# Optimization experiments

Measured on AMD Instinct MI355X. Metric: run time of the kernel, lower is better.

The kernel has to match this reference:

```python
import jax, jax.numpy as jnp
import numpy as np

N, E, G = 10000, 160000, 64
F, C1, C2, C3, K, NC = 128, 128, 256, 512, 5, 10


def setup_inputs() -> dict:
    key = jax.random.key(0)
    ks = jax.random.split(key, 12)
    s = 0.05
    return {
        "x": jax.random.normal(ks[0], (N, F), dtype=jnp.float32),
        "edge_index": jax.random.randint(ks[1], (2, E), 0, N, dtype=jnp.int64),
        "batch": jnp.sort(jax.random.randint(ks[2], (N,), 0, G, dtype=jnp.int64)),
        "W_cheb": jax.random.normal(ks[3], (K, F, C1), dtype=jnp.float32) * s,
        "b_cheb": jnp.zeros((C1,), jnp.float32),
        "W_g1": jax.random.normal(ks[4], (C1, C2), dtype=jnp.float32) * s,
        "b_g1": jnp.zeros((C2,), jnp.float32),
        "W_g2": jax.random.normal(ks[5], (C2, C3), dtype=jnp.float32) * s,
        "b_g2": jnp.zeros((C3,), jnp.float32),
        "w_gate": jax.random.normal(ks[6], (C3, 1), dtype=jnp.float32) * s,
        "b_gate": jnp.zeros((1,), jnp.float32),
        "W_fc": jax.random.normal(ks[7], (C3, NC), dtype=jnp.float32) * s,
        "b_fc": jnp.zeros((NC,), jnp.float32),
    }


def _deg_inv_sqrt(deg):
    return jnp.where(deg > 0, jax.lax.rsqrt(jnp.maximum(deg, 1e-12)), 0.0)


def cheb_conv(x, src, dst, W, b):
    # PyG ChebConv, sym normalization, lambda_max=2 => scaled Laplacian = -D^-1/2 A D^-1/2
    ones = jnp.ones((src.shape[0],), x.dtype)
    deg = jax.ops.segment_sum(ones, src, num_segments=N)
    dinv = _deg_inv_sqrt(deg)
    w = -(dinv[src] * dinv[dst])  # [E]

    def prop(h):
        return jax.ops.segment_sum(w[:, None] * h[src], dst, num_segments=N)

    tx0 = x
    tx1 = prop(x)
    out = tx0 @ W[0] + tx1 @ W[1]
    for k in range(2, W.shape[0]):
        tx2 = 2.0 * prop(tx1) - tx0
        out = out + tx2 @ W[k]
        tx0, tx1 = tx1, tx2
    return out + b


def gcn_conv(x, src, dst, W, b):
    # PyG GCNConv: add self-loops, sym norm D~^-1/2 (A+I) D~^-1/2, transform then aggregate
    loop = jnp.arange(N, dtype=src.dtype)
    src_a = jnp.concatenate([src, loop])
    dst_a = jnp.concatenate([dst, loop])
    ones = jnp.ones((src_a.shape[0],), x.dtype)
    deg = jax.ops.segment_sum(ones, dst_a, num_segments=N)
    dinv = _deg_inv_sqrt(deg)
    norm = dinv[src_a] * dinv[dst_a]  # [E+N]
    h = x @ W
    return jax.ops.segment_sum(norm[:, None] * h[src_a], dst_a, num_segments=N) + b


def attention_pool(x, batch, w_gate, b_gate):
    logits = (x @ w_gate + b_gate)[:, 0]  # [N]
    m = jax.ops.segment_max(logits, batch, num_segments=G)
    e = jnp.exp(logits - m[batch])
    s = jax.ops.segment_sum(e, batch, num_segments=G)
    alpha = e / s[batch]
    return jax.ops.segment_sum(alpha[:, None] * x, batch, num_segments=G)  # [G, C3]


def reference(x, edge_index, batch, W_cheb, b_cheb, W_g1, b_g1, W_g2, b_g2,
              w_gate, b_gate, W_fc, b_fc):
    src, dst = edge_index[0], edge_index[1]
    h = jax.nn.relu(cheb_conv(x, src, dst, W_cheb, b_cheb))
    h = jax.nn.relu(gcn_conv(h, src, dst, W_g1, b_g1))
    h = jax.nn.relu(gcn_conv(h, src, dst, W_g2, b_g2))
    g = attention_pool(h, batch, w_gate, b_gate)
    logits = g @ W_fc + b_fc
    return jax.nn.log_softmax(logits, axis=1)
```

## Files before the change

### kernel.cpp

```cpp
#include <hip/hip_runtime.h>
#include <hip/hip_bf16.h>
#include <math.h>

#define N_NODES 10000
#define N_EDGES 160000
#define N_GRAPHS 64
#define F_IN    128
#define C1_DIM  128
#define C2_DIM  256
#define C3_DIM  512
#define K_CHEB  5
#define NCLS    10
#define TC      (K_CHEB * F_IN)

typedef short v8s __attribute__((ext_vector_type(8)));
typedef float v4f __attribute__((ext_vector_type(4)));

static __device__ __forceinline__ unsigned short f2bf(float f) {
    unsigned u = __float_as_uint(f);
    unsigned r = (u + 0x7FFFu + ((u >> 16) & 1u)) >> 16;
    return (unsigned short)r;
}
static __device__ __forceinline__ float bf_lo(unsigned u) { return __uint_as_float(u << 16); }
static __device__ __forceinline__ float bf_hi(unsigned u) { return __uint_as_float(u & 0xFFFF0000u); }

#define PREP_A (N_NODES * 32)
#define PREP_B (TC * C1_DIM)
#define PREP_C (C1_DIM * C2_DIM)
#define PREP_D (C2_DIM * C3_DIM)
#define PREP_E N_NODES
#define PREP_F N_NODES
#define PREP_H (N_GRAPHS * C3_DIM)
#define PREP_G N_EDGES
#define PREP_TOTAL (PREP_A + PREP_B + PREP_C + PREP_D + PREP_E + PREP_F + PREP_H + PREP_G)
__global__ void prep_kernel(const float* __restrict__ x, unsigned short* __restrict__ tcat,
                            const float* __restrict__ Wcheb, unsigned short* __restrict__ Wcb_t,
                            const float* __restrict__ Wg1, unsigned short* __restrict__ Wg1_t,
                            const float* __restrict__ Wg2, unsigned short* __restrict__ Wg2_t,
                            const int* __restrict__ batch, int* __restrict__ gptr,
                            float* __restrict__ logits, float* __restrict__ pooled,
                            const int* __restrict__ src, const int* __restrict__ dst,
                            int* __restrict__ cnt_s, int* __restrict__ cnt_d) {
    int id = blockIdx.x * blockDim.x + threadIdx.x;
    if (id < PREP_A) {
        int n = id >> 5, f = (id & 31) * 4;
        float4 v = *(const float4*)(x + (size_t)n * F_IN + f);
        ushort4 o; o.x = f2bf(v.x); o.y = f2bf(v.y); o.z = f2bf(v.z); o.w = f2bf(v.w);
        *(ushort4*)(tcat + (size_t)n * TC + f) = o;
        return;
    }
    id -= PREP_A;
    if (id < PREP_B) {
        int k = id % TC, n = id / TC;
        Wcb_t[(size_t)n * TC + k] = f2bf(Wcheb[(size_t)k * C1_DIM + n]);
        return;
    }
    id -= PREP_B;
    if (id < PREP_C) {
        int k = id % C1_DIM, n = id / C1_DIM;
        Wg1_t[(size_t)n * C1_DIM + k] = f2bf(Wg1[(size_t)k * C2_DIM + n]);
        return;
    }
    id -= PREP_C;
    if (id < PREP_D) {
        int k = id % C2_DIM, n = id / C2_DIM;
        Wg2_t[(size_t)n * C2_DIM + k] = f2bf(Wg2[(size_t)k * C3_DIM + n]);
        return;
    }
    id -= PREP_D;
    if (id < PREP_E) {
        int i = id;
        int b = batch[i];
        if (i == 0) { for (int g = 0; g <= b; g++) gptr[g] = 0; }
        else {
            int bp = batch[i - 1];
            for (int g = bp + 1; g <= b; g++) gptr[g] = i;
        }
        if (i == N_NODES - 1) { for (int g = b + 1; g <= N_GRAPHS; g++) gptr[g] = N_NODES; }
        return;
    }
    id -= PREP_E;
    if (id < PREP_F) { logits[id] = 0.0f; return; }
    id -= PREP_F;
    if (id < PREP_H) { pooled[id] = 0.0f; return; }
    id -= PREP_H;
    if (id < PREP_G) {
        atomicAdd(&cnt_s[src[id]], 1);
        atomicAdd(&cnt_d[dst[id]], 1);
    }
}

__global__ __launch_bounds__(256) void scan_kernel(const int* __restrict__ cnt_d,
                                                   int* __restrict__ rowptr, int n) {
    __shared__ int ldsc[N_NODES];
    __shared__ int sums[256];
    int tid = threadIdx.x;
    for (int i = tid; i < n; i += 256) ldsc[i] = cnt_d[i];
    __syncthreads();
    int chunk = (n + 255) / 256;
    int s0 = min(n, tid * chunk), s1 = min(n, s0 + chunk);
    int loc = 0;
    for (int i = s0; i < s1; i++) loc += ldsc[i];
    sums[tid] = loc;
    __syncthreads();
    for (int off = 1; off < 256; off <<= 1) {
        int t = (tid >= off) ? sums[tid - off] : 0;
        __syncthreads();
        sums[tid] += t;
        __syncthreads();
    }
    int pre = sums[tid] - loc;
    for (int i = s0; i < s1; i++) { int v = ldsc[i]; ldsc[i] = pre; pre += v; }
    __syncthreads();
    for (int i = tid; i < n; i += 256) rowptr[i] = ldsc[i];
    if (tid == 255) rowptr[n] = pre;
}

__global__ void fill_kernel(const int* __restrict__ src, const int* __restrict__ dst,
                            const int* __restrict__ cnt_s, const int* __restrict__ cnt_d,
                            const int* __restrict__ rowptr, int* __restrict__ fillc,
                            int2* __restrict__ ecb, int2* __restrict__ egc, int E) {
    int e = blockIdx.x * blockDim.x + threadIdx.x;
    if (e >= E) return;
    int s = src[e], d = dst[e];
    int pos = rowptr[d] + atomicAdd(&fillc[d], 1);
    int cs = cnt_s[s], cd = cnt_s[d];
    float ds = (cs > 0) ? rsqrtf((float)cs) : 0.0f;
    float dd = (cd > 0) ? rsqrtf((float)cd) : 0.0f;
    float nr = rsqrtf((float)cnt_d[s] + 1.0f) * rsqrtf((float)cnt_d[d] + 1.0f);
    ecb[pos] = make_int2(s, __float_as_int(-(ds * dd)));
    egc[pos] = make_int2(s, __float_as_int(nr));
}

__global__ __launch_bounds__(256) void gather_cheb_bf(
        const unsigned short* __restrict__ tb, const int* __restrict__ rowptr,
        const int2* __restrict__ edges,
        const unsigned short* __restrict__ base, float alpha, float beta,
        unsigned short* __restrict__ outc, int n) {
    int w = (blockIdx.x * blockDim.x + threadIdx.x) >> 6;
    int lane = threadIdx.x & 63;
    if (w >= n) return;
    float a0 = 0.0f, a1 = 0.0f;
    int rs = rowptr[w], re = rowptr[w + 1];
    for (int b = rs; b < re; b += 64) {
        int cl = 0; float wl = 0.0f;
        if (b + lane < re) { int2 e = edges[b + lane]; cl = e.x; wl = __int_as_float(e.y); }
        int nk16 = (min(64, re - b) + 15) & ~15;
        for (int j = 0; j < nk16; j += 16) {
            int ss[16]; float ww[16]; unsigned uu[16];
            #pragma unroll
            for (int q = 0; q < 16; q++) { ss[q] = __shfl(cl, j + q); ww[q] = __shfl(wl, j + q); }
            #pragma unroll
            for (int q = 0; q < 16; q++) uu[q] = ((const unsigned*)(tb + (size_t)ss[q] * TC))[lane];
            #pragma unroll
            for (int q = 0; q < 16; q++) { a0 += ww[q] * bf_lo(uu[q]); a1 += ww[q] * bf_hi(uu[q]); }
        }
    }
    if (base) {
        unsigned ub = ((const unsigned*)(base + (size_t)w * TC))[lane];
        a0 = alpha * a0 + beta * bf_lo(ub);
        a1 = alpha * a1 + beta * bf_hi(ub);
    } else {
        a0 *= alpha; a1 *= alpha;
    }
    ushort2 o; o.x = f2bf(a0); o.y = f2bf(a1);
    *(ushort2*)(outc + (size_t)w * TC + lane * 2) = o;
}

template<int FPL>
__global__ __launch_bounds__(256) void gather_gcn_pre(
        const unsigned short* __restrict__ tb, const int* __restrict__ rowptr,
        const int2* __restrict__ edges,
        const int* __restrict__ cnt_d, unsigned short* __restrict__ z, int n) {
    const int C = FPL * 64;
    int w = (blockIdx.x * blockDim.x + threadIdx.x) >> 6;
    int lane = threadIdx.x & 63;
    if (w >= n) return;
    float acc[FPL];
    #pragma unroll
    for (int q = 0; q < FPL; q++) acc[q] = 0.0f;
    int rs = rowptr[w], re = rowptr[w + 1];
    for (int b = rs; b < re; b += 64) {
        int cl = 0; float wl = 0.0f;
        if (b + lane < re) { int2 e = edges[b + lane]; cl = e.x; wl = __int_as_float(e.y); }
        int nk16 = (min(64, re - b) + 15) & ~15;
        for (int j = 0; j < nk16; j += 16) {
            int ss[16]; float ww[16];
            #pragma unroll
            for (int q = 0; q < 16; q++) { ss[q] = __shfl(cl, j + q); ww[q] = __shfl(wl, j + q); }
            if constexpr (FPL == 2) {
                unsigned uu[16];
                #pragma unroll
                for (int q = 0; q < 16; q++) uu[q] = ((const unsigned*)(tb + (size_t)ss[q] * C))[lane];
                #pragma unroll
                for (int q = 0; q < 16; q++) { acc[0] += ww[q] * bf_lo(uu[q]); acc[1] += ww[q] * bf_hi(uu[q]); }
            } else {
                uint2 uu[16];
                #pragma unroll
                for (int q = 0; q < 16; q++) uu[q] = ((const uint2*)(tb + (size_t)ss[q] * C))[lane];
                #pragma unroll
                for (int q = 0; q < 16; q++) {
                    acc[0] += ww[q] * bf_lo(uu[q].x); acc[1] += ww[q] * bf_hi(uu[q].x);
                    acc[2] += ww[q] * bf_lo(uu[q].y); acc[3] += ww[q] * bf_hi(uu[q].y);
                }
            }
        }
    }
    float sn = 1.0f / (float)(cnt_d[w] + 1);
    if constexpr (FPL == 2) {
        unsigned u = ((const unsigned*)(tb + (size_t)w * C))[lane];
        acc[0] += sn * bf_lo(u); acc[1] += sn * bf_hi(u);
        ushort2 o; o.x = f2bf(acc[0]); o.y = f2bf(acc[1]);
        *(ushort2*)(z + (size_t)w * C + lane * 2) = o;
    } else {
        uint2 u = ((const uint2*)(tb + (size_t)w * C))[lane];
        acc[0] += sn * bf_lo(u.x); acc[1] += sn * bf_hi(u.x);
        acc[2] += sn * bf_lo(u.y); acc[3] += sn * bf_hi(u.y);
        ushort4 o; o.x = f2bf(acc[0]); o.y = f2bf(acc[1]);
        o.z = f2bf(acc[2]); o.w = f2bf(acc[3]);
        *(ushort4*)(z + (size_t)w * C + lane * 4) = o;
    }
}

template<int JT, int KC>
__global__ __launch_bounds__(256) void gemm_bf16(
        const unsigned short* __restrict__ A, const unsigned short* __restrict__ Bt,
        const float* __restrict__ bias,
        unsigned short* __restrict__ Cb, const float* __restrict__ wg,
        float* __restrict__ logits, int M, int N) {
    int m0 = blockIdx.y * 64, n0 = blockIdx.x * (JT * 32);
    int wave = threadIdx.x >> 6, lane = threadIdx.x & 63;
    int wm = (wave & 1) * 32, wn = (wave >> 1) * (JT * 16);
    int l15 = lane & 15, quad = lane >> 4;

    v4f acc[2][JT];
    #pragma unroll
    for (int i = 0; i < 2; i++)
        #pragma unroll
        for (int j = 0; j < JT; j++) acc[i][j] = (v4f){0.f, 0.f, 0.f, 0.f};

    const unsigned short* Ab[2]; bool av[2];
    #pragma unroll
    for (int i = 0; i < 2; i++) {
        int row = m0 + wm + i * 16 + l15;
        av[i] = row < M;
        Ab[i] = A + (size_t)(av[i] ? row : 0) * KC + quad * 8;
    }
    const unsigned short* Bb[JT];
    #pragma unroll
    for (int j = 0; j < JT; j++) {
        int coln = n0 + wn + j * 16 + l15;
        Bb[j] = Bt + (size_t)coln * KC + quad * 8;
    }
    const v8s zero8 = {0, 0, 0, 0, 0, 0, 0, 0};

    #pragma unroll
    for (int k0 = 0; k0 < KC; k0 += 32) {
        v8s a[2], b[JT];
        #pragma unroll
        for (int i = 0; i < 2; i++) a[i] = av[i] ? *(const v8s*)(Ab[i] + k0) : zero8;
        #pragma unroll
        for (int j = 0; j < JT; j++) b[j] = *(const v8s*)(Bb[j] + k0);
        #pragma unroll
        for (int i = 0; i < 2; i++)
            #pragma unroll
            for (int j = 0; j < JT; j++)
                acc[i][j] = __builtin_amdgcn_mfma_f32_16x16x32_bf16(a[i], b[j], acc[i][j], 0, 0, 0);
    }

    float bv[JT], wgj[JT];
    #pragma unroll
    for (int j = 0; j < JT; j++) {
        int coln = n0 + wn + j * 16 + l15;
        bv[j] = bias[coln];
        wgj[j] = wg ? wg[coln] : 0.0f;
    }
    #pragma unroll
    for (int i = 0; i < 2; i++) {
        #pragma unroll
        for (int r = 0; r < 4; r++) {
            int row = m0 + wm + i * 16 + quad * 4 + r;
            if (row >= M) continue;
            float gval = 0.0f;
            #pragma unroll
            for (int j = 0; j < JT; j++) {
                int coln = n0 + wn + j * 16 + l15;
                float v = fmaxf(acc[i][j][r] + bv[j], 0.0f);
                Cb[(size_t)row * N + coln] = f2bf(v);
                gval += v * wgj[j];
            }
            if (wg) {
                #pragma unroll
                for (int off = 1; off < 16; off <<= 1) gval += __shfl_xor(gval, off);
                if (l15 == 0) atomicAdd(&logits[row], gval);
            }
        }
    }
}

__global__ __launch_bounds__(256) void pool_partial(const unsigned short* __restrict__ h3b,
        const float* __restrict__ logits, const int* __restrict__ gptr,
        float* __restrict__ pooled) {
    __shared__ float red[256];
    int g = blockIdx.x, sl = blockIdx.y, tid = threadIdx.x;
    int gs = gptr[g], ge = gptr[g + 1];
    float m = -INFINITY;
    for (int i = gs + tid; i < ge; i += 256) m = fmaxf(m, logits[i]);
    red[tid] = m; __syncthreads();
    for (int off = 128; off > 0; off >>= 1) {
        if (tid < off) red[tid] = fmaxf(red[tid], red[tid + off]);
        __syncthreads();
    }
    m = red[0]; __syncthreads();
    float s = 0.0f;
    for (int i = gs + tid; i < ge; i += 256) s += expf(logits[i] - m);
    red[tid] = s; __syncthreads();
    for (int off = 128; off > 0; off >>= 1) {
        if (tid < off) red[tid] += red[tid + off];
        __syncthreads();
    }
    s = red[0];
    float sinv = (s > 0.0f) ? 1.0f / s : 0.0f;
    int cnt = ge - gs;
    int i0 = gs + (cnt * sl) / 8;
    int i1 = gs + (cnt * (sl + 1)) / 8;
    float a0 = 0.0f, a1 = 0.0f;
    for (int i = i0; i < i1; i++) {
        float al = expf(logits[i] - m) * sinv;
        unsigned u = ((const unsigned*)(h3b + (size_t)i * C3_DIM))[tid];
        a0 += al * bf_lo(u);
        a1 += al * bf_hi(u);
    }
    if (i1 > i0) {
        atomicAdd(&pooled[(size_t)g * C3_DIM + tid * 2 + 0], a0);
        atomicAdd(&pooled[(size_t)g * C3_DIM + tid * 2 + 1], a1);
    }
}

__global__ void fc_kernel(const float* __restrict__ pooled, const float* __restrict__ Wfc,
                          const float* __restrict__ bfc, float* __restrict__ out) {
    int g = blockIdx.x;
    int t = threadIdx.x;
    float acc = -INFINITY;
    if (t < NCLS) {
        acc = bfc[t];
        for (int k = 0; k < C3_DIM; k++)
            acc += pooled[(size_t)g * C3_DIM + k] * Wfc[k * NCLS + t];
    }
    float m = acc;
    #pragma unroll
    for (int off = 8; off > 0; off >>= 1) m = fmaxf(m, __shfl_xor(m, off, 16));
    float e = (t < NCLS) ? expf(acc - m) : 0.0f;
    float s = e;
    #pragma unroll
    for (int off = 8; off > 0; off >>= 1) s += __shfl_xor(s, off, 16);
    if (t < NCLS) out[g * NCLS + t] = acc - m - logf(s);
}

extern "C" void kernel_launch(void* const* d_in, const int* in_sizes, int n_in,
                              void* d_out, int out_size, void* d_ws, size_t ws_size,
                              hipStream_t stream) {
    const float* x      = (const float*)d_in[0];
    const int*   ei     = (const int*)d_in[1];
    const int*   batch  = (const int*)d_in[2];
    const float* W_cheb = (const float*)d_in[3];
    const float* b_cheb = (const float*)d_in[4];
    const float* W_g1   = (const float*)d_in[5];
    const float* b_g1   = (const float*)d_in[6];
    const float* W_g2   = (const float*)d_in[7];
    const float* b_g2   = (const float*)d_in[8];
    const float* w_gate = (const float*)d_in[9];
    const float* W_fc   = (const float*)d_in[11];
    const float* b_fc   = (const float*)d_in[12];
    const int* src = ei;
    const int* dst = ei + N_EDGES;
    float* out = (float*)d_out;

    const int N = N_NODES, E = N_EDGES, G = N_GRAPHS;

    char* Wp = (char*)d_ws;
    auto alloc = [&](size_t bytes) {
        void* p = Wp;
        Wp += (bytes + 255) & ~(size_t)255;
        return p;
    };
    int*   cnt3    = (int*)alloc((size_t)3 * N * 4);
    int*   cnt_s   = cnt3;
    int*   cnt_d   = cnt3 + N;
    int*   fillc   = cnt3 + 2 * N;
    int*   rowptr  = (int*)alloc((N + 1) * 4);
    int2*  ecb     = (int2*)alloc((size_t)E * 8);
    int2*  egc     = (int2*)alloc((size_t)E * 8);
    unsigned short* tcat  = (unsigned short*)alloc((size_t)N * TC * 2);
    unsigned short* h1b   = (unsigned short*)alloc((size_t)N * C1_DIM * 2);
    unsigned short* z1b   = (unsigned short*)alloc((size_t)N * C1_DIM * 2);
    unsigned short* h2b   = (unsigned short*)alloc((size_t)N * C2_DIM * 2);
    unsigned short* z2b   = (unsigned short*)alloc((size_t)N * C2_DIM * 2);
    unsigned short* h3b   = (unsigned short*)alloc((size_t)N * C3_DIM * 2);
    unsigned short* Wcb_t = (unsigned short*)alloc((size_t)TC * C1_DIM * 2);
    unsigned short* Wg1_t = (unsigned short*)alloc((size_t)C1_DIM * C2_DIM * 2);
    unsigned short* Wg2_t = (unsigned short*)alloc((size_t)C2_DIM * C3_DIM * 2);
    float* logits  = (float*)alloc(N * 4);
    int*   gptr    = (int*)alloc((G + 1) * 4);
    float* pooled  = (float*)alloc((size_t)G * C3_DIM * 4);

    dim3 blk(256);
    auto cdiv = [](int a, int b) { return (a + b - 1) / b; };

    hipMemsetAsync(cnt3, 0, (size_t)3 * N * sizeof(int), stream);
    hipLaunchKernelGGL(prep_kernel, dim3(cdiv(PREP_TOTAL, 256)), blk, 0, stream,
                       x, tcat, W_cheb, Wcb_t, W_g1, Wg1_t, W_g2, Wg2_t,
                       batch, gptr, logits, pooled, src, dst, cnt_s, cnt_d);

    hipLaunchKernelGGL(scan_kernel, dim3(1), blk, 0, stream, cnt_d, rowptr, N);
    hipLaunchKernelGGL(fill_kernel, dim3(cdiv(E, 256)), blk, 0, stream,
                       src, dst, cnt_s, cnt_d, rowptr, fillc, ecb, egc, E);

    const int NWB = cdiv(N, 4);

    hipLaunchKernelGGL(gather_cheb_bf, dim3(NWB), blk, 0, stream,
                       tcat + 0 * F_IN, rowptr, ecb,
                       (const unsigned short*)nullptr, 1.0f, 0.0f, tcat + 1 * F_IN, N);
    hipLaunchKernelGGL(gather_cheb_bf, dim3(NWB), blk, 0, stream,
                       tcat + 1 * F_IN, rowptr, ecb,
                       tcat + 0 * F_IN, 2.0f, -1.0f, tcat + 2 * F_IN, N);
    hipLaunchKernelGGL(gather_cheb_bf, dim3(NWB), blk, 0, stream,
                       tcat + 2 * F_IN, rowptr, ecb,
                       tcat + 1 * F_IN, 2.0f, -1.0f, tcat + 3 * F_IN, N);
    hipLaunchKernelGGL(gather_cheb_bf, dim3(NWB), blk, 0, stream,
                       tcat + 3 * F_IN, rowptr, ecb,
                       tcat + 2 * F_IN, 2.0f, -1.0f, tcat + 4 * F_IN, N);

    hipLaunchKernelGGL((gemm_bf16<2, TC>), dim3(C1_DIM / 64, cdiv(N, 64)), blk, 0, stream,
                       tcat, Wcb_t, b_cheb, h1b,
                       (const float*)nullptr, (float*)nullptr, N, C1_DIM);

    hipLaunchKernelGGL(gather_gcn_pre<2>, dim3(NWB), blk, 0, stream,
                       h1b, rowptr, egc, cnt_d, z1b, N);
    hipLaunchKernelGGL((gemm_bf16<4, C1_DIM>), dim3(C2_DIM / 128, cdiv(N, 64)), blk, 0, stream,
                       z1b, Wg1_t, b_g1, h2b,
                       (const float*)nullptr, (float*)nullptr, N, C2_DIM);

    hipLaunchKernelGGL(gather_gcn_pre<4>, dim3(NWB), blk, 0, stream,
                       h2b, rowptr, egc, cnt_d, z2b, N);
    hipLaunchKernelGGL((gemm_bf16<4, C2_DIM>), dim3(C3_DIM / 128, cdiv(N, 64)), blk, 0, stream,
                       z2b, Wg2_t, b_g2, h3b,
                       w_gate, logits, N, C3_DIM);

    hipLaunchKernelGGL(pool_partial, dim3(G, 8), blk, 0, stream, h3b, logits, gptr, pooled);
    hipLaunchKernelGGL(fc_kernel, dim3(G), dim3(64), 0, stream, pooled, W_fc, b_fc, out);
}
```

Measured before the change: 264.1 us.

## Fuse graph gathers into following GEMMs via LDS and merge pool with FC

Each aggregation step (the last Chebyshev propagation and both GCN neighbour sums) now runs inside the GEMM kernel that consumes it. The aggregated 64-row tile is written to LDS and fed to the MFMA loop from there, so the intermediate z1/z2 buffers and the fourth Chebyshev slice never go to global memory. Attention pooling and the FC/log-softmax are merged into one kernel with one block per graph, which removes the pooled atomics and their zeroing. In exchange each GEMM block now covers the full output width and does the irregular gather serially per wave, giving fewer blocks (157) and lower parallelism, and the pooling no longer splits a graph's nodes across 8 blocks.

```diff
diff --git a/kernel.cpp b/kernel.cpp
--- a/kernel.cpp
+++ b/kernel.cpp
@@ -12,6 +12,8 @@
 #define K_CHEB  5
 #define NCLS    10
 #define TC      (K_CHEB * F_IN)
+#define LDSW1   136
+#define LDSW2   264
 
 typedef short v8s __attribute__((ext_vector_type(8)));
 typedef float v4f __attribute__((ext_vector_type(4)));
@@ -30,15 +32,14 @@
 #define PREP_D (C2_DIM * C3_DIM)
 #define PREP_E N_NODES
 #define PREP_F N_NODES
-#define PREP_H (N_GRAPHS * C3_DIM)
 #define PREP_G N_EDGES
-#define PREP_TOTAL (PREP_A + PREP_B + PREP_C + PREP_D + PREP_E + PREP_F + PREP_H + PREP_G)
+#define PREP_TOTAL (PREP_A + PREP_B + PREP_C + PREP_D + PREP_E + PREP_F + PREP_G)
 __global__ void prep_kernel(const float* __restrict__ x, unsigned short* __restrict__ tcat,
                             const float* __restrict__ Wcheb, unsigned short* __restrict__ Wcb_t,
                             const float* __restrict__ Wg1, unsigned short* __restrict__ Wg1_t,
                             const float* __restrict__ Wg2, unsigned short* __restrict__ Wg2_t,
                             const int* __restrict__ batch, int* __restrict__ gptr,
-                            float* __restrict__ logits, float* __restrict__ pooled,
+                            float* __restrict__ logits,
                             const int* __restrict__ src, const int* __restrict__ dst,
                             int* __restrict__ cnt_s, int* __restrict__ cnt_d) {
     int id = blockIdx.x * blockDim.x + threadIdx.x;
@@ -82,8 +83,6 @@
     id -= PREP_E;
     if (id < PREP_F) { logits[id] = 0.0f; return; }
     id -= PREP_F;
-    if (id < PREP_H) { pooled[id] = 0.0f; return; }
-    id -= PREP_H;
     if (id < PREP_G) {
         atomicAdd(&cnt_s[src[id]], 1);
         atomicAdd(&cnt_d[dst[id]], 1);
@@ -167,113 +166,256 @@
     *(ushort2*)(outc + (size_t)w * TC + lane * 2) = o;
 }
 
-template<int FPL>
-__global__ __launch_bounds__(256) void gather_gcn_pre(
-        const unsigned short* __restrict__ tb, const int* __restrict__ rowptr,
-        const int2* __restrict__ edges,
-        const int* __restrict__ cnt_d, unsigned short* __restrict__ z, int n) {
-    const int C = FPL * 64;
-    int w = (blockIdx.x * blockDim.x + threadIdx.x) >> 6;
-    int lane = threadIdx.x & 63;
-    if (w >= n) return;
-    float acc[FPL];
-    #pragma unroll
-    for (int q = 0; q < FPL; q++) acc[q] = 0.0f;
-    int rs = rowptr[w], re = rowptr[w + 1];
-    for (int b = rs; b < re; b += 64) {
-        int cl = 0; float wl = 0.0f;
-        if (b + lane < re) { int2 e = edges[b + lane]; cl = e.x; wl = __int_as_float(e.y); }
-        int nk16 = (min(64, re - b) + 15) & ~15;
-        for (int j = 0; j < nk16; j += 16) {
-            int ss[16]; float ww[16];
-            #pragma unroll
-            for (int q = 0; q < 16; q++) { ss[q] = __shfl(cl, j + q); ww[q] = __shfl(wl, j + q); }
-            if constexpr (FPL == 2) {
-                unsigned uu[16];
-                #pragma unroll
-                for (int q = 0; q < 16; q++) uu[q] = ((const unsigned*)(tb + (size_t)ss[q] * C))[lane];
-                #pragma unroll
-                for (int q = 0; q < 16; q++) { acc[0] += ww[q] * bf_lo(uu[q]); acc[1] += ww[q] * bf_hi(uu[q]); }
-            } else {
-                uint2 uu[16];
-                #pragma unroll
-                for (int q = 0; q < 16; q++) uu[q] = ((const uint2*)(tb + (size_t)ss[q] * C))[lane];
-                #pragma unroll
-                for (int q = 0; q < 16; q++) {
-                    acc[0] += ww[q] * bf_lo(uu[q].x); acc[1] += ww[q] * bf_hi(uu[q].x);
-                    acc[2] += ww[q] * bf_lo(uu[q].y); acc[3] += ww[q] * bf_hi(uu[q].y);
+__global__ __launch_bounds__(256) void cheb4_gemm1(
+        const unsigned short* __restrict__ tcat, const int* __restrict__ rowptr,
+        const int2* __restrict__ ecb, const unsigned short* __restrict__ Bt,
+        const float* __restrict__ bias, unsigned short* __restrict__ h1b, int M) {
+    __shared__ unsigned short ldsA[64 * LDSW1];
+    int tid = threadIdx.x, wave = tid >> 6, lane = tid & 63;
+    int m0 = blockIdx.x * 64;
+    const unsigned short* t3 = tcat + 3 * F_IN;
+    const unsigned short* t2 = tcat + 2 * F_IN;
+
+    for (int na = wave * 16; na < wave * 16 + 16; na++) {
+        int w = m0 + na;
+        float a0 = 0.0f, a1 = 0.0f;
+        if (w < M) {
+            int rs = rowptr[w], re = rowptr[w + 1];
+            for (int b = rs; b < re; b += 64) {
+                int cl = 0; float wl = 0.0f;
+                if (b + lane < re) { int2 e = ecb[b + lane]; cl = e.x; wl = __int_as_float(e.y); }
+                int nk16 = (min(64, re - b) + 15) & ~15;
+                for (int j = 0; j < nk16; j += 16) {
+                    int ss[16]; float ww[16]; unsigned uu[16];
+                    #pragma unroll
+                    for (int q = 0; q < 16; q++) { ss[q] = __shfl(cl, j + q); ww[q] = __shfl(wl, j + q); }
+                    #pragma unroll
+                    for (int q = 0; q < 16; q++) uu[q] = ((const unsigned*)(t3 + (size_t)ss[q] * TC))[lane];
+                    #pragma unroll
+                    for (int q = 0; q < 16; q++) { a0 += ww[q] * bf_lo(uu[q]); a1 += ww[q] * bf_hi(uu[q]); }
                 }
             }
-        }
-    }
-    float sn = 1.0f / (float)(cnt_d[w] + 1);
-    if constexpr (FPL == 2) {
-        unsigned u = ((const unsigned*)(tb + (size_t)w * C))[lane];
-        acc[0] += sn * bf_lo(u); acc[1] += sn * bf_hi(u);
-        ushort2 o; o.x = f2bf(acc[0]); o.y = f2bf(acc[1]);
-        *(ushort2*)(z + (size_t)w * C + lane * 2) = o;
-    } else {
-        uint2 u = ((const uint2*)(tb + (size_t)w * C))[lane];
-        acc[0] += sn * bf_lo(u.x); acc[1] += sn * bf_hi(u.x);
-        acc[2] += sn * bf_lo(u.y); acc[3] += sn * bf_hi(u.y);
-        ushort4 o; o.x = f2bf(acc[0]); o.y = f2bf(acc[1]);
-        o.z = f2bf(acc[2]); o.w = f2bf(acc[3]);
-        *(ushort4*)(z + (size_t)w * C + lane * 4) = o;
-    }
-}
-
-template<int JT, int KC>
-__global__ __launch_bounds__(256) void gemm_bf16(
-        const unsigned short* __restrict__ A, const unsigned short* __restrict__ Bt,
-        const float* __restrict__ bias,
-        unsigned short* __restrict__ Cb, const float* __restrict__ wg,
-        float* __restrict__ logits, int M, int N) {
-    int m0 = blockIdx.y * 64, n0 = blockIdx.x * (JT * 32);
-    int wave = threadIdx.x >> 6, lane = threadIdx.x & 63;
-    int wm = (wave & 1) * 32, wn = (wave >> 1) * (JT * 16);
+            unsigned ub = ((const unsigned*)(t2 + (size_t)w * TC))[lane];
+            a0 = 2.0f * a0 - bf_lo(ub);
+            a1 = 2.0f * a1 - bf_hi(ub);
+        }
+        ushort2 o; o.x = f2bf(a0); o.y = f2bf(a1);
+        *(ushort2*)(ldsA + na * LDSW1 + lane * 2) = o;
+    }
+    __syncthreads();
+
+    int wm = (wave & 1) * 32, wn = (wave >> 1) * 64;
     int l15 = lane & 15, quad = lane >> 4;
-
-    v4f acc[2][JT];
+    v4f acc[2][4];
     #pragma unroll
     for (int i = 0; i < 2; i++)
         #pragma unroll
-        for (int j = 0; j < JT; j++) acc[i][j] = (v4f){0.f, 0.f, 0.f, 0.f};
-
-    const unsigned short* Ab[2]; bool av[2];
+        for (int j = 0; j < 4; j++) acc[i][j] = (v4f){0.f, 0.f, 0.f, 0.f};
+    const unsigned short* Ab[2]; bool av[2]; int rl[2];
     #pragma unroll
     for (int i = 0; i < 2; i++) {
         int row = m0 + wm + i * 16 + l15;
         av[i] = row < M;
-        Ab[i] = A + (size_t)(av[i] ? row : 0) * KC + quad * 8;
-    }
-    const unsigned short* Bb[JT];
-    #pragma unroll
-    for (int j = 0; j < JT; j++) {
-        int coln = n0 + wn + j * 16 + l15;
-        Bb[j] = Bt + (size_t)coln * KC + quad * 8;
+        Ab[i] = tcat + (size_t)(av[i] ? row : 0) * TC + quad * 8;
+        rl[i] = wm + i * 16 + l15;
+    }
+    const unsigned short* Bb[4];
+    #pragma unroll
+    for (int j = 0; j < 4; j++) {
+        int coln = wn + j * 16 + l15;
+        Bb[j] = Bt + (size_t)coln * TC + quad * 8;
     }
     const v8s zero8 = {0, 0, 0, 0, 0, 0, 0, 0};
-
-    #pragma unroll
-    for (int k0 = 0; k0 < KC; k0 += 32) {
-        v8s a[2], b[JT];
-        #pragma unroll
-        for (int i = 0; i < 2; i++) a[i] = av[i] ? *(const v8s*)(Ab[i] + k0) : zero8;
-        #pragma unroll
-        for (int j = 0; j < JT; j++) b[j] = *(const v8s*)(Bb[j] + k0);
+    #pragma unroll
+    for (int k0 = 0; k0 < TC; k0 += 32) {
+        v8s a[2], b[4];
+        #pragma unroll
+        for (int i = 0; i < 2; i++) {
+            if (k0 < 4 * F_IN) a[i] = av[i] ? *(const v8s*)(Ab[i] + k0) : zero8;
+            else               a[i] = *(const v8s*)(ldsA + rl[i] * LDSW1 + (k0 - 4 * F_IN) + quad * 8);
+        }
+        #pragma unroll
+        for (int j = 0; j < 4; j++) b[j] = *(const v8s*)(Bb[j] + k0);
         #pragma unroll
         for (int i = 0; i < 2; i++)
             #pragma unroll
-            for (int j = 0; j < JT; j++)
+            for (int j = 0; j < 4; j++)
                 acc[i][j] = __builtin_amdgcn_mfma_f32_16x16x32_bf16(a[i], b[j], acc[i][j], 0, 0, 0);
     }
-
-    float bv[JT], wgj[JT];
-    #pragma unroll
-    for (int j = 0; j < JT; j++) {
-        int coln = n0 + wn + j * 16 + l15;
+    #pragma unroll
+    for (int j = 0; j < 4; j++) {
+        int coln = wn + j * 16 + l15;
+        float bv = bias[coln];
+        #pragma unroll
+        for (int i = 0; i < 2; i++) {
+            #pragma unroll
+            for (int r = 0; r < 4; r++) {
+                int row = m0 + wm + i * 16 + quad * 4 + r;
+                if (row >= M) continue;
+                float v = fmaxf(acc[i][j][r] + bv, 0.0f);
+                h1b[(size_t)row * C1_DIM + coln] = f2bf(v);
+            }
+        }
+    }
+}
+
+__global__ __launch_bounds__(256) void gcn_gemm2(
+        const unsigned short* __restrict__ h1b, const int* __restrict__ rowptr,
+        const int2* __restrict__ egc, const int* __restrict__ cnt_d,
+        const unsigned short* __restrict__ Bt, const float* __restrict__ bias,
+        unsigned short* __restrict__ h2b, int M) {
+    __shared__ unsigned short ldsA[64 * LDSW1];
+    int tid = threadIdx.x, wave = tid >> 6, lane = tid & 63;
+    int m0 = blockIdx.x * 64;
+
+    for (int na = wave * 16; na < wave * 16 + 16; na++) {
+        int w = m0 + na;
+        float a0 = 0.0f, a1 = 0.0f;
+        if (w < M) {
+            int rs = rowptr[w], re = rowptr[w + 1];
+            for (int b = rs; b < re; b += 64) {
+                int cl = 0; float wl = 0.0f;
+                if (b + lane < re) { int2 e = egc[b + lane]; cl = e.x; wl = __int_as_float(e.y); }
+                int nk16 = (min(64, re - b) + 15) & ~15;
+                for (int j = 0; j < nk16; j += 16) {
+                    int ss[16]; float ww[16]; unsigned uu[16];
+                    #pragma unroll
+                    for (int q = 0; q < 16; q++) { ss[q] = __shfl(cl, j + q); ww[q] = __shfl(wl, j + q); }
+                    #pragma unroll
+                    for (int q = 0; q < 16; q++) uu[q] = ((const unsigned*)(h1b + (size_t)ss[q] * C1_DIM))[lane];
+                    #pragma unroll
+                    for (int q = 0; q < 16; q++) { a0 += ww[q] * bf_lo(uu[q]); a1 += ww[q] * bf_hi(uu[q]); }
+                }
+            }
+            float sn = 1.0f / (float)(cnt_d[w] + 1);
+            unsigned u = ((const unsigned*)(h1b + (size_t)w * C1_DIM))[lane];
+            a0 += sn * bf_lo(u);
+            a1 += sn * bf_hi(u);
+        }
+        ushort2 o; o.x = f2bf(a0); o.y = f2bf(a1);
+        *(ushort2*)(ldsA + na * LDSW1 + lane * 2) = o;
+    }
+    __syncthreads();
+
+    int wm = (wave & 1) * 32, wn = (wave >> 1) * 128;
+    int l15 = lane & 15, quad = lane >> 4;
+    v4f acc[2][8];
+    #pragma unroll
+    for (int i = 0; i < 2; i++)
+        #pragma unroll
+        for (int j = 0; j < 8; j++) acc[i][j] = (v4f){0.f, 0.f, 0.f, 0.f};
+    int rl[2] = {wm + l15, wm + 16 + l15};
+    const unsigned short* Bb[8];
+    #pragma unroll
+    for (int j = 0; j < 8; j++) {
+        int coln = wn + j * 16 + l15;
+        Bb[j] = Bt + (size_t)coln * C1_DIM + quad * 8;
+    }
+    #pragma unroll
+    for (int k0 = 0; k0 < C1_DIM; k0 += 32) {
+        v8s a[2], b[8];
+        #pragma unroll
+        for (int i = 0; i < 2; i++) a[i] = *(const v8s*)(ldsA + rl[i] * LDSW1 + k0 + quad * 8);
+        #pragma unroll
+        for (int j = 0; j < 8; j++) b[j] = *(const v8s*)(Bb[j] + k0);
+        #pragma unroll
+        for (int i = 0; i < 2; i++)
+            #pragma unroll
+            for (int j = 0; j < 8; j++)
+                acc[i][j] = __builtin_amdgcn_mfma_f32_16x16x32_bf16(a[i], b[j], acc[i][j], 0, 0, 0);
+    }
+    #pragma unroll
+    for (int j = 0; j < 8; j++) {
+        int coln = wn + j * 16 + l15;
+        float bv = bias[coln];
+        #pragma unroll
+        for (int i = 0; i < 2; i++) {
+            #pragma unroll
+            for (int r = 0; r < 4; r++) {
+                int row = m0 + wm + i * 16 + quad * 4 + r;
+                if (row >= M) continue;
+                float v = fmaxf(acc[i][j][r] + bv, 0.0f);
+                h2b[(size_t)row * C2_DIM + coln] = f2bf(v);
+            }
+        }
+    }
+}
+
+__global__ __launch_bounds__(512) void gcn_gemm3(
+        const unsigned short* __restrict__ h2b, const int* __restrict__ rowptr,
+        const int2* __restrict__ egc, const int* __restrict__ cnt_d,
+        const unsigned short* __restrict__ Bt, const float* __restrict__ bias,
+        const float* __restrict__ wg, unsigned short* __restrict__ h3b,
+        float* __restrict__ logits, int M) {
+    __shared__ unsigned short ldsA[64 * LDSW2];
+    int tid = threadIdx.x, wave = tid >> 6, lane = tid & 63;
+    int m0 = blockIdx.x * 64;
+
+    for (int na = wave * 8; na < wave * 8 + 8; na++) {
+        int w = m0 + na;
+        float a0 = 0.0f, a1 = 0.0f, a2 = 0.0f, a3 = 0.0f;
+        if (w < M) {
+            int rs = rowptr[w], re = rowptr[w + 1];
+            for (int b = rs; b < re; b += 64) {
+                int cl = 0; float wl = 0.0f;
+                if (b + lane < re) { int2 e = egc[b + lane]; cl = e.x; wl = __int_as_float(e.y); }
+                int nk16 = (min(64, re - b) + 15) & ~15;
+                for (int j = 0; j < nk16; j += 16) {
+                    int ss[16]; float ww[16]; uint2 uu[16];
+                    #pragma unroll
+                    for (int q = 0; q < 16; q++) { ss[q] = __shfl(cl, j + q); ww[q] = __shfl(wl, j + q); }
+                    #pragma unroll
+                    for (int q = 0; q < 16; q++) uu[q] = ((const uint2*)(h2b + (size_t)ss[q] * C2_DIM))[lane];
+                    #pragma unroll
+                    for (int q = 0; q < 16; q++) {
+                        a0 += ww[q] * bf_lo(uu[q].x); a1 += ww[q] * bf_hi(uu[q].x);
+                        a2 += ww[q] * bf_lo(uu[q].y); a3 += ww[q] * bf_hi(uu[q].y);
+                    }
+                }
+            }
+            float sn = 1.0f / (float)(cnt_d[w] + 1);
+            uint2 u = ((const uint2*)(h2b + (size_t)w * C2_DIM))[lane];
+            a0 += sn * bf_lo(u.x); a1 += sn * bf_hi(u.x);
+            a2 += sn * bf_lo(u.y); a3 += sn * bf_hi(u.y);
+        }
+        ushort4 o; o.x = f2bf(a0); o.y = f2bf(a1); o.z = f2bf(a2); o.w = f2bf(a3);
+        *(ushort4*)(ldsA + na * LDSW2 + lane * 4) = o;
+    }
+    __syncthreads();
+
+    int wm = (wave >> 2) * 32, wn = (wave & 3) * 128;
+    int l15 = lane & 15, quad = lane >> 4;
+    v4f acc[2][8];
+    #pragma unroll
+    for (int i = 0; i < 2; i++)
+        #pragma unroll
+        for (int j = 0; j < 8; j++) acc[i][j] = (v4f){0.f, 0.f, 0.f, 0.f};
+    int rl[2] = {wm + l15, wm + 16 + l15};
+    const unsigned short* Bb[8];
+    #pragma unroll
+    for (int j = 0; j < 8; j++) {
+        int coln = wn + j * 16 + l15;
+        Bb[j] = Bt + (size_t)coln * C2_DIM + quad * 8;
+    }
+    #pragma unroll
+    for (int k0 = 0; k0 < C2_DIM; k0 += 32) {
+        v8s a[2], b[8];
+        #pragma unroll
+        for (int i = 0; i < 2; i++) a[i] = *(const v8s*)(ldsA + rl[i] * LDSW2 + k0 + quad * 8);
+        #pragma unroll
+        for (int j = 0; j < 8; j++) b[j] = *(const v8s*)(Bb[j] + k0);
+        #pragma unroll
+        for (int i = 0; i < 2; i++)
+            #pragma unroll
+            for (int j = 0; j < 8; j++)
+                acc[i][j] = __builtin_amdgcn_mfma_f32_16x16x32_bf16(a[i], b[j], acc[i][j], 0, 0, 0);
+    }
+    float bv[8], wgj[8];
+    #pragma unroll
+    for (int j = 0; j < 8; j++) {
+        int coln = wn + j * 16 + l15;
         bv[j] = bias[coln];
-        wgj[j] = wg ? wg[coln] : 0.0f;
+        wgj[j] = wg[coln];
     }
     #pragma unroll
     for (int i = 0; i < 2; i++) {
@@ -283,26 +425,26 @@
             if (row >= M) continue;
             float gval = 0.0f;
             #pragma unroll
-            for (int j = 0; j < JT; j++) {
-                int coln = n0 + wn + j * 16 + l15;
+            for (int j = 0; j < 8; j++) {
+                int coln = wn + j * 16 + l15;
                 float v = fmaxf(acc[i][j][r] + bv[j], 0.0f);
-                Cb[(size_t)row * N + coln] = f2bf(v);
+                h3b[(size_t)row * C3_DIM + coln] = f2bf(v);
                 gval += v * wgj[j];
             }
-            if (wg) {
-                #pragma unroll
-                for (int off = 1; off < 16; off <<= 1) gval += __shfl_xor(gval, off);
-                if (l15 == 0) atomicAdd(&logits[row], gval);
-            }
-        }
-    }
-}
-
-__global__ __launch_bounds__(256) void pool_partial(const unsigned short* __restrict__ h3b,
+            #pragma unroll
+            for (int off = 1; off < 16; off <<= 1) gval += __shfl_xor(gval, off);
+            if (l15 == 0) atomicAdd(&logits[row], gval);
+        }
+    }
+}
+
+__global__ __launch_bounds__(256) void pool_fc(const unsigned short* __restrict__ h3b,
         const float* __restrict__ logits, const int* __restrict__ gptr,
-        float* __restrict__ pooled) {
+        const float* __restrict__ Wfc, const float* __restrict__ bfc,
+        float* __restrict__ out) {
     __shared__ float red[256];
-    int g = blockIdx.x, sl = blockIdx.y, tid = threadIdx.x;
+    __shared__ float plds[C3_DIM];
+    int g = blockIdx.x, tid = threadIdx.x;
     int gs = gptr[g], ge = gptr[g + 1];
     float m = -INFINITY;
     for (int i = gs + tid; i < ge; i += 256) m = fmaxf(m, logits[i]);
@@ -321,40 +463,32 @@
     }
     s = red[0];
     float sinv = (s > 0.0f) ? 1.0f / s : 0.0f;
-    int cnt = ge - gs;
-    int i0 = gs + (cnt * sl) / 8;
-    int i1 = gs + (cnt * (sl + 1)) / 8;
     float a0 = 0.0f, a1 = 0.0f;
-    for (int i = i0; i < i1; i++) {
+    for (int i = gs; i < ge; i++) {
         float al = expf(logits[i] - m) * sinv;
         unsigned u = ((const unsigned*)(h3b + (size_t)i * C3_DIM))[tid];
         a0 += al * bf_lo(u);
         a1 += al * bf_hi(u);
     }
-    if (i1 > i0) {
-        atomicAdd(&pooled[(size_t)g * C3_DIM + tid * 2 + 0], a0);
-        atomicAdd(&pooled[(size_t)g * C3_DIM + tid * 2 + 1], a1);
-    }
-}
-
-__global__ void fc_kernel(const float* __restrict__ pooled, const float* __restrict__ Wfc,
-                          const float* __restrict__ bfc, float* __restrict__ out) {
-    int g = blockIdx.x;
-    int t = threadIdx.x;
-    float acc = -INFINITY;
-    if (t < NCLS) {
-        acc = bfc[t];
-        for (int k = 0; k < C3_DIM; k++)
-            acc += pooled[(size_t)g * C3_DIM + k] * Wfc[k * NCLS + t];
-    }
-    float m = acc;
-    #pragma unroll
-    for (int off = 8; off > 0; off >>= 1) m = fmaxf(m, __shfl_xor(m, off, 16));
-    float e = (t < NCLS) ? expf(acc - m) : 0.0f;
-    float s = e;
-    #pragma unroll
-    for (int off = 8; off > 0; off >>= 1) s += __shfl_xor(s, off, 16);
-    if (t < NCLS) out[g * NCLS + t] = acc - m - logf(s);
+    plds[tid * 2 + 0] = a0;
+    plds[tid * 2 + 1] = a1;
+    __syncthreads();
+    if (tid < 16) {
+        float acc = -INFINITY;
+        if (tid < NCLS) {
+            acc = bfc[tid];
+            for (int k = 0; k < C3_DIM; k++)
+                acc += plds[k] * Wfc[k * NCLS + tid];
+        }
+        float mm = acc;
+        #pragma unroll
+        for (int off = 8; off > 0; off >>= 1) mm = fmaxf(mm, __shfl_xor(mm, off, 16));
+        float e = (tid < NCLS) ? expf(acc - mm) : 0.0f;
+        float ss = e;
+        #pragma unroll
+        for (int off = 8; off > 0; off >>= 1) ss += __shfl_xor(ss, off, 16);
+        if (tid < NCLS) out[g * NCLS + tid] = acc - mm - logf(ss);
+    }
 }
 
 extern "C" void kernel_launch(void* const* d_in, const int* in_sizes, int n_in,
@@ -393,16 +527,13 @@
     int2*  egc     = (int2*)alloc((size_t)E * 8);
     unsigned short* tcat  = (unsigned short*)alloc((size_t)N * TC * 2);
     unsigned short* h1b   = (unsigned short*)alloc((size_t)N * C1_DIM * 2);
-    unsigned short* z1b   = (unsigned short*)alloc((size_t)N * C1_DIM * 2);
     unsigned short* h2b   = (unsigned short*)alloc((size_t)N * C2_DIM * 2);
-    unsigned short* z2b   = (unsigned short*)alloc((size_t)N * C2_DIM * 2);
     unsigned short* h3b   = (unsigned short*)alloc((size_t)N * C3_DIM * 2);
     unsigned short* Wcb_t = (unsigned short*)alloc((size_t)TC * C1_DIM * 2);
     unsigned short* Wg1_t = (unsigned short*)alloc((size_t)C1_DIM * C2_DIM * 2);
     unsigned short* Wg2_t = (unsigned short*)alloc((size_t)C2_DIM * C3_DIM * 2);
     float* logits  = (float*)alloc(N * 4);
     int*   gptr    = (int*)alloc((G + 1) * 4);
-    float* pooled  = (float*)alloc((size_t)G * C3_DIM * 4);
 
     dim3 blk(256);
     auto cdiv = [](int a, int b) { return (a + b - 1) / b; };
@@ -410,7 +541,7 @@
     hipMemsetAsync(cnt3, 0, (size_t)3 * N * sizeof(int), stream);
     hipLaunchKernelGGL(prep_kernel, dim3(cdiv(PREP_TOTAL, 256)), blk, 0, stream,
                        x, tcat, W_cheb, Wcb_t, W_g1, Wg1_t, W_g2, Wg2_t,
-                       batch, gptr, logits, pooled, src, dst, cnt_s, cnt_d);
+                       batch, gptr, logits, src, dst, cnt_s, cnt_d);
 
     hipLaunchKernelGGL(scan_kernel, dim3(1), blk, 0, stream, cnt_d, rowptr, N);
     hipLaunchKernelGGL(fill_kernel, dim3(cdiv(E, 256)), blk, 0, stream,
@@ -427,26 +558,16 @@
     hipLaunchKernelGGL(gather_cheb_bf, dim3(NWB), blk, 0, stream,
                        tcat + 2 * F_IN, rowptr, ecb,
                        tcat + 1 * F_IN, 2.0f, -1.0f, tcat + 3 * F_IN, N);
-    hipLaunchKernelGGL(gather_cheb_bf, dim3(NWB), blk, 0, stream,
-                       tcat + 3 * F_IN, rowptr, ecb,
-                       tcat + 2 * F_IN, 2.0f, -1.0f, tcat + 4 * F_IN, N);
-
-    hipLaunchKernelGGL((gemm_bf16<2, TC>), dim3(C1_DIM / 64, cdiv(N, 64)), blk, 0, stream,
-                       tcat, Wcb_t, b_cheb, h1b,
-                       (const float*)nullptr, (float*)nullptr, N, C1_DIM);
-
-    hipLaunchKernelGGL(gather_gcn_pre<2>, dim3(NWB), blk, 0, stream,
-                       h1b, rowptr, egc, cnt_d, z1b, N);
-    hipLaunchKernelGGL((gemm_bf16<4, C1_DIM>), dim3(C2_DIM / 128, cdiv(N, 64)), blk, 0, stream,
-                       z1b, Wg1_t, b_g1, h2b,
-                       (const float*)nullptr, (float*)nullptr, N, C2_DIM);
-
-    hipLaunchKernelGGL(gather_gcn_pre<4>, dim3(NWB), blk, 0, stream,
-                       h2b, rowptr, egc, cnt_d, z2b, N);
-    hipLaunchKernelGGL((gemm_bf16<4, C2_DIM>), dim3(C3_DIM / 128, cdiv(N, 64)), blk, 0, stream,
-                       z2b, Wg2_t, b_g2, h3b,
-                       w_gate, logits, N, C3_DIM);
-
-    hipLaunchKernelGGL(pool_partial, dim3(G, 8), blk, 0, stream, h3b, logits, gptr, pooled);
-    hipLaunchKernelGGL(fc_kernel, dim3(G), dim3(64), 0, stream, pooled, W_fc, b_fc, out);
-}
+
+    hipLaunchKernelGGL(cheb4_gemm1, dim3(cdiv(N, 64)), blk, 0, stream,
+                       tcat, rowptr, ecb, Wcb_t, b_cheb, h1b, N);
+
+    hipLaunchKernelGGL(gcn_gemm2, dim3(cdiv(N, 64)), blk, 0, stream,
+                       h1b, rowptr, egc, cnt_d, Wg1_t, b_g1, h2b, N);
+
+    hipLaunchKernelGGL(gcn_gemm3, dim3(cdiv(N, 64)), dim3(512), 0, stream,
+                       h2b, rowptr, egc, cnt_d, Wg2_t, b_g2, w_gate, h3b, logits, N);
+
+    hipLaunchKernelGGL(pool_fc, dim3(G), blk, 0, stream,
+                       h3b, logits, gptr, W_fc, b_fc, out);
+}
```

Result: slower. 339.9 us (+28.7%).

## Fuse scan into fill kernel and fuse pooling with FC via last-block counter

Applied to the files above, without the earlier changes.

The single-block prefix scan is folded into the edge fill kernel: every block redundantly scans the 10000 degree counts in LDS, and block 0 writes rowptr. Separately, the FC and log-softmax are merged into the pooling kernel using a per-graph atomic completion counter, so the last of the 8 slice blocks finishes each graph. This removes two kernel launches and the serial gap of a one-block scan kernel. In exchange, 625 blocks each repeat the 10K-element scan and the pool tail adds threadfence and atomic overhead.

```diff
diff --git a/kernel.cpp b/kernel.cpp
--- a/kernel.cpp
+++ b/kernel.cpp
@@ -31,14 +31,16 @@
 #define PREP_E N_NODES
 #define PREP_F N_NODES
 #define PREP_H (N_GRAPHS * C3_DIM)
+#define PREP_I N_GRAPHS
 #define PREP_G N_EDGES
-#define PREP_TOTAL (PREP_A + PREP_B + PREP_C + PREP_D + PREP_E + PREP_F + PREP_H + PREP_G)
+#define PREP_TOTAL (PREP_A + PREP_B + PREP_C + PREP_D + PREP_E + PREP_F + PREP_H + PREP_I + PREP_G)
 __global__ void prep_kernel(const float* __restrict__ x, unsigned short* __restrict__ tcat,
                             const float* __restrict__ Wcheb, unsigned short* __restrict__ Wcb_t,
                             const float* __restrict__ Wg1, unsigned short* __restrict__ Wg1_t,
                             const float* __restrict__ Wg2, unsigned short* __restrict__ Wg2_t,
                             const int* __restrict__ batch, int* __restrict__ gptr,
                             float* __restrict__ logits, float* __restrict__ pooled,
+                            int* __restrict__ gdone,
                             const int* __restrict__ src, const int* __restrict__ dst,
                             int* __restrict__ cnt_s, int* __restrict__ cnt_d) {
     int id = blockIdx.x * blockDim.x + threadIdx.x;
@@ -84,14 +86,19 @@
     id -= PREP_F;
     if (id < PREP_H) { pooled[id] = 0.0f; return; }
     id -= PREP_H;
+    if (id < PREP_I) { gdone[id] = 0; return; }
+    id -= PREP_I;
     if (id < PREP_G) {
         atomicAdd(&cnt_s[src[id]], 1);
         atomicAdd(&cnt_d[dst[id]], 1);
     }
 }
 
-__global__ __launch_bounds__(256) void scan_kernel(const int* __restrict__ cnt_d,
-                                                   int* __restrict__ rowptr, int n) {
+__global__ __launch_bounds__(256) void fill_scan_kernel(
+        const int* __restrict__ src, const int* __restrict__ dst,
+        const int* __restrict__ cnt_s, const int* __restrict__ cnt_d,
+        int* __restrict__ rowptr, int* __restrict__ fillc,
+        int2* __restrict__ ecb, int2* __restrict__ egc, int E, int n) {
     __shared__ int ldsc[N_NODES];
     __shared__ int sums[256];
     int tid = threadIdx.x;
@@ -112,18 +119,14 @@
     int pre = sums[tid] - loc;
     for (int i = s0; i < s1; i++) { int v = ldsc[i]; ldsc[i] = pre; pre += v; }
     __syncthreads();
-    for (int i = tid; i < n; i += 256) rowptr[i] = ldsc[i];
-    if (tid == 255) rowptr[n] = pre;
-}
-
-__global__ void fill_kernel(const int* __restrict__ src, const int* __restrict__ dst,
-                            const int* __restrict__ cnt_s, const int* __restrict__ cnt_d,
-                            const int* __restrict__ rowptr, int* __restrict__ fillc,
-                            int2* __restrict__ ecb, int2* __restrict__ egc, int E) {
-    int e = blockIdx.x * blockDim.x + threadIdx.x;
+    if (blockIdx.x == 0) {
+        for (int i = tid; i < n; i += 256) rowptr[i] = ldsc[i];
+        if (tid == 255) rowptr[n] = pre;
+    }
+    int e = blockIdx.x * 256 + tid;
     if (e >= E) return;
     int s = src[e], d = dst[e];
-    int pos = rowptr[d] + atomicAdd(&fillc[d], 1);
+    int pos = ldsc[d] + atomicAdd(&fillc[d], 1);
     int cs = cnt_s[s], cd = cnt_s[d];
     float ds = (cs > 0) ? rsqrtf((float)cs) : 0.0f;
     float dd = (cd > 0) ? rsqrtf((float)cd) : 0.0f;
@@ -298,10 +301,14 @@
     }
 }
 
-__global__ __launch_bounds__(256) void pool_partial(const unsigned short* __restrict__ h3b,
+__global__ __launch_bounds__(256) void pool_fc_fused(const unsigned short* __restrict__ h3b,
         const float* __restrict__ logits, const int* __restrict__ gptr,
-        float* __restrict__ pooled) {
+        float* __restrict__ pooled, int* __restrict__ gdone,
+        const float* __restrict__ Wfc, const float* __restrict__ bfc,
+        float* __restrict__ out) {
     __shared__ float red[256];
+    __shared__ float plds[C3_DIM];
+    __shared__ int lastf;
     int g = blockIdx.x, sl = blockIdx.y, tid = threadIdx.x;
     int gs = gptr[g], ge = gptr[g + 1];
     float m = -INFINITY;
@@ -335,26 +342,30 @@
         atomicAdd(&pooled[(size_t)g * C3_DIM + tid * 2 + 0], a0);
         atomicAdd(&pooled[(size_t)g * C3_DIM + tid * 2 + 1], a1);
     }
-}
-
-__global__ void fc_kernel(const float* __restrict__ pooled, const float* __restrict__ Wfc,
-                          const float* __restrict__ bfc, float* __restrict__ out) {
-    int g = blockIdx.x;
-    int t = threadIdx.x;
-    float acc = -INFINITY;
-    if (t < NCLS) {
-        acc = bfc[t];
-        for (int k = 0; k < C3_DIM; k++)
-            acc += pooled[(size_t)g * C3_DIM + k] * Wfc[k * NCLS + t];
-    }
-    float m = acc;
-    #pragma unroll
-    for (int off = 8; off > 0; off >>= 1) m = fmaxf(m, __shfl_xor(m, off, 16));
-    float e = (t < NCLS) ? expf(acc - m) : 0.0f;
-    float s = e;
-    #pragma unroll
-    for (int off = 8; off > 0; off >>= 1) s += __shfl_xor(s, off, 16);
-    if (t < NCLS) out[g * NCLS + t] = acc - m - logf(s);
+    __threadfence();
+    __syncthreads();
+    if (tid == 0) lastf = (atomicAdd(&gdone[g], 1) == 7) ? 1 : 0;
+    __syncthreads();
+    if (!lastf) return;
+    plds[tid * 2 + 0] = atomicAdd(&pooled[(size_t)g * C3_DIM + tid * 2 + 0], 0.0f);
+    plds[tid * 2 + 1] = atomicAdd(&pooled[(size_t)g * C3_DIM + tid * 2 + 1], 0.0f);
+    __syncthreads();
+    if (tid < 16) {
+        float acc = -INFINITY;
+        if (tid < NCLS) {
+            acc = bfc[tid];
+            for (int k = 0; k < C3_DIM; k++)
+                acc += plds[k] * Wfc[k * NCLS + tid];
+        }
+        float mm = acc;
+        #pragma unroll
+        for (int off = 8; off > 0; off >>= 1) mm = fmaxf(mm, __shfl_xor(mm, off, 16));
+        float e = (tid < NCLS) ? expf(acc - mm) : 0.0f;
+        float ss = e;
+        #pragma unroll
+        for (int off = 8; off > 0; off >>= 1) ss += __shfl_xor(ss, off, 16);
+        if (tid < NCLS) out[g * NCLS + tid] = acc - mm - logf(ss);
+    }
 }
 
 extern "C" void kernel_launch(void* const* d_in, const int* in_sizes, int n_in,
@@ -403,6 +414,7 @@
     float* logits  = (float*)alloc(N * 4);
     int*   gptr    = (int*)alloc((G + 1) * 4);
     float* pooled  = (float*)alloc((size_t)G * C3_DIM * 4);
+    int*   gdone   = (int*)alloc(G * 4);
 
     dim3 blk(256);
     auto cdiv = [](int a, int b) { return (a + b - 1) / b; };
@@ -410,11 +422,10 @@
     hipMemsetAsync(cnt3, 0, (size_t)3 * N * sizeof(int), stream);
     hipLaunchKernelGGL(prep_kernel, dim3(cdiv(PREP_TOTAL, 256)), blk, 0, stream,
                        x, tcat, W_cheb, Wcb_t, W_g1, Wg1_t, W_g2, Wg2_t,
-                       batch, gptr, logits, pooled, src, dst, cnt_s, cnt_d);
-
-    hipLaunchKernelGGL(scan_kernel, dim3(1), blk, 0, stream, cnt_d, rowptr, N);
-    hipLaunchKernelGGL(fill_kernel, dim3(cdiv(E, 256)), blk, 0, stream,
-                       src, dst, cnt_s, cnt_d, rowptr, fillc, ecb, egc, E);
+                       batch, gptr, logits, pooled, gdone, src, dst, cnt_s, cnt_d);
+
+    hipLaunchKernelGGL(fill_scan_kernel, dim3(cdiv(E, 256)), blk, 0, stream,
+                       src, dst, cnt_s, cnt_d, rowptr, fillc, ecb, egc, E, N);
 
     const int NWB = cdiv(N, 4);
 
@@ -447,6 +458,6 @@
                        z2b, Wg2_t, b_g2, h3b,
                        w_gate, logits, N, C3_DIM);
 
-    hipLaunchKernelGGL(pool_partial, dim3(G, 8), blk, 0, stream, h3b, logits, gptr, pooled);
-    hipLaunchKernelGGL(fc_kernel, dim3(G), dim3(64), 0, stream, pooled, W_fc, b_fc, out);
-}
+    hipLaunchKernelGGL(pool_fc_fused, dim3(G, 8), blk, 0, stream,
+                       h3b, logits, gptr, pooled, gdone, W_fc, b_fc, out);
+}
```

Result: slower. 290.9 us (+10.1%).
